# Optimization experiments

Measured on AMD Instinct MI355X. Metric: run time of the kernel, lower is better.

Reference implementation:

```python
import jax, jax.numpy as jnp
import numpy as np

IMAGE_SIZE = 128
FACES_PER_PIXEL = 4
BLUR_RADIUS = 0.01
EPS = 1e-8


def setup_inputs() -> dict:
    key = jax.random.key(0)
    k1, k2, k3 = jax.random.split(key, 3)
    B, V, F = 2, 2000, 800
    # verts are already projected to screen/NDC space: x,y in [-1,1], z > 0 (depth)
    xy = jax.random.uniform(k1, (B, V, 2), minval=-1.0, maxval=1.0)
    z = jax.random.uniform(k2, (B, V, 1), minval=0.5, maxval=2.5)
    verts = jnp.concatenate([xy, z], axis=-1).astype(jnp.float32)
    faces = jax.random.randint(k3, (F, 3), 0, V)
    return {"verts": verts, "faces": faces}


def _edge(a, b, p):
    # signed parallelogram area of (a -> b -> p), using xy components only
    return (p[..., 0] - a[..., 0]) * (b[..., 1] - a[..., 1]) - (
        p[..., 1] - a[..., 1]) * (b[..., 0] - a[..., 0])


def _seg_dist2(p, a, b):
    # squared distance from point p to segment [a, b] in 2D
    ab = b - a
    pa = p - a
    t = jnp.clip(jnp.sum(pa * ab, -1) / (jnp.sum(ab * ab, -1) + EPS), 0.0, 1.0)
    d = pa - t[..., None] * ab
    return jnp.sum(d * d, -1)


def _rasterize(verts, faces):
    H = W = IMAGE_SIZE
    K = FACES_PER_PIXEL
    B = verts.shape[0]
    fv = verts[:, faces]                      # [B,F,3,3] gather face vertices
    v0, v1, v2 = fv[:, :, 0], fv[:, :, 1], fv[:, :, 2]
    a0 = v0[:, None, :, :2]                   # [B,1,F,2]
    a1 = v1[:, None, :, :2]
    a2 = v2[:, None, :, :2]
    z0 = v0[:, None, :, 2]                    # [B,1,F]
    z1 = v1[:, None, :, 2]
    z2 = v2[:, None, :, 2]
    # pixel centers in NDC, pytorch3d convention: index 0 -> +1, last -> -1
    xs = 1.0 - 2.0 * (jnp.arange(W, dtype=verts.dtype) + 0.5) / W
    ys = 1.0 - 2.0 * (jnp.arange(H, dtype=verts.dtype) + 0.5) / H
    yy, xx = jnp.meshgrid(ys, xs, indexing="ij")
    p = jnp.stack([xx, yy], -1).reshape(1, -1, 1, 2)   # [1,P,1,2], P=H*W

    area = _edge(a0, a1, a2)                  # [B,1,F] signed face area*2
    w0 = _edge(a1, a2, p)                     # [B,P,F]
    w1 = _edge(a2, a0, p)
    w2 = _edge(a0, a1, p)
    denom = jnp.where(jnp.abs(area) > EPS, area,
                      jnp.where(area >= 0, EPS, -EPS))
    b0, b1, b2 = w0 / denom, w1 / denom, w2 / denom
    zpix = b0 * z0 + b1 * z1 + b2 * z2        # [B,P,F] interpolated depth

    inside = (b0 >= 0) & (b1 >= 0) & (b2 >= 0)
    dmin = jnp.minimum(_seg_dist2(p, a0, a1),
                       jnp.minimum(_seg_dist2(p, a1, a2),
                                   _seg_dist2(p, a2, a0)))
    dsign = jnp.where(inside, -dmin, dmin)    # signed squared edge distance

    valid = (inside | (dmin < BLUR_RADIUS)) & (zpix > EPS) & (
        jnp.abs(area) > EPS)
    zcand = jnp.where(valid, zpix, jnp.inf)
    _, idx = jax.lax.top_k(-zcand, K)         # K nearest faces per pixel

    take = lambda x: jnp.take_along_axis(x, idx, axis=-1)
    sel_valid = take(valid)
    pix_to_face = jnp.where(sel_valid, idx, -1)
    zbuf = jnp.where(sel_valid, take(zpix), -1.0)
    bary = jnp.stack([b0, b1, b2], -1)        # [B,P,F,3]
    bsel = jnp.take_along_axis(bary, idx[..., None], axis=2)  # [B,P,K,3]
    bsel = jnp.where(sel_valid[..., None], bsel, -1.0)
    dsel = jnp.where(sel_valid, take(dsign), -1.0)

    return (pix_to_face.reshape(B, H, W, K),
            zbuf.reshape(B, H, W, K),
            bsel.reshape(B, H, W, K, 3),
            dsel.reshape(B, H, W, K))


def reference(verts, faces):
    # Fragments: (pix_to_face, zbuf, bary_coords, dists)
    return _rasterize(verts, faces)
```

## Files before the change

kernel.cpp:

```cpp
#include <hip/hip_runtime.h>

#define IMG   128
#define KF    4
#define NF    800
#define NV    2000
#define NB    2
#define EPSF  1e-8f
#define BLURF 0.01f
#define CULL_D2 0.0103f
#define HEXT    0.0547f

typedef unsigned long long u64;
#define INVK ((((u64)0x7f800000u) << 32) | 0xffffffffu)

#pragma clang fp contract(off)

__device__ __forceinline__ float rcp2(float d) {
    float y = __builtin_amdgcn_rcpf(d);
    float e = __builtin_fmaf(-d, y, 1.0f);
    y = __builtin_fmaf(y, e, y);
    e = __builtin_fmaf(-d, y, 1.0f);
    y = __builtin_fmaf(y, e, y);
    return y;
}
__device__ __forceinline__ float fdivr(float n, float d, float y) {
    float q0 = n * y;
    float r  = __builtin_fmaf(-d, q0, n);
    return __builtin_fmaf(r, y, q0);
}

__device__ __forceinline__ float seg_d2(float pax, float pay, float abx, float aby) {
#pragma clang fp contract(off)
    float dd = (abx * abx + aby * aby) + EPSF;
    float t  = (pax * abx + pay * aby) / dd;
    t = fminf(fmaxf(t, 0.0f), 1.0f);
    float dx = pax - t * abx;
    float dy = pay - t * aby;
    return dx * dx + dy * dy;
}

__device__ __forceinline__ float seg_d2f(float pax, float pay, float abx, float aby) {
#pragma clang fp contract(off)
    float dd = (abx * abx + aby * aby) + EPSF;
    float n  = pax * abx + pay * aby;
    float y  = rcp2(dd);
    float t  = fdivr(n, dd, y);
    t = fminf(fmaxf(t, 0.0f), 1.0f);
    float dx = pax - t * abx;
    float dy = pay - t * aby;
    return dx * dx + dy * dy;
}

__device__ __forceinline__ void ins4(u64& s0, u64& s1, u64& s2, u64& s3, u64 k) {
    bool c0 = k < s0, c1 = k < s1, c2 = k < s2, c3 = k < s3;
    s3 = c2 ? s2 : (c3 ? k : s3);
    s2 = c1 ? s1 : (c2 ? k : s2);
    s1 = c0 ? s0 : (c1 ? k : s1);
    s0 = c0 ? k  : s0;
}

__global__ __launch_bounds__(256) void raster_p1(
    const float* __restrict__ verts,
    const int*   __restrict__ faces,
    u64* __restrict__ ws,
    int sh)
{
#pragma clang fp contract(off)
    extern __shared__ float sFD[];
    __shared__ u64 sK[2 * 4 * 64];
    __shared__ int sTot;

    const int S     = 1 << sh;
    const int chunk = NF >> sh;

    const int tid   = threadIdx.x;
    const int blk   = blockIdx.x;
    const int tile  = blk >> sh;
    const int slice = blk & (S - 1);
    const int b     = tile >> 8;
    const int trow  = (tile & 255) >> 4;
    const int tcol  = tile & 15;
    const float* vb = verts + b * NV * 3;
    const int fbase = slice * chunk;

    if (tid == 0) sTot = 0;

    const float txmax = 1.0f - (2.0f * ((float)(tcol * 8)     + 0.5f)) / 128.0f;
    const float txmin = 1.0f - (2.0f * ((float)(tcol * 8 + 7) + 0.5f)) / 128.0f;
    const float tymax = 1.0f - (2.0f * ((float)(trow * 8)     + 0.5f)) / 128.0f;
    const float tymin = 1.0f - (2.0f * ((float)(trow * 8 + 7) + 0.5f)) / 128.0f;
    const float cx = 0.5f * (txmin + txmax);
    const float cy = 0.5f * (tymin + tymax);

    __syncthreads();

    for (int j = tid; j < chunk; j += 256) {
        int f = fbase + j;
        int i0 = faces[3 * f + 0], i1 = faces[3 * f + 1], i2 = faces[3 * f + 2];
        float a0x = vb[3 * i0], a0y = vb[3 * i0 + 1], z0 = vb[3 * i0 + 2];
        float a1x = vb[3 * i1], a1y = vb[3 * i1 + 1], z1 = vb[3 * i1 + 2];
        float a2x = vb[3 * i2], a2y = vb[3 * i2 + 1], z2 = vb[3 * i2 + 2];
        float area = (a2x - a0x) * (a1y - a0y) - (a2y - a0y) * (a1x - a0x);
        bool surv = fabsf(area) > EPSF;
        float bxmin = fminf(a0x, fminf(a1x, a2x)) - 0.101f;
        float bxmax = fmaxf(a0x, fmaxf(a1x, a2x)) + 0.101f;
        float bymin = fminf(a0y, fminf(a1y, a2y)) - 0.101f;
        float bymax = fmaxf(a0y, fmaxf(a1y, a2y)) + 0.101f;
        surv &= !(bxmin > txmax || bxmax < txmin || bymin > tymax || bymax < tymin);
        float s = (area >= 0.0f) ? 1.0f : -1.0f;
        float e0x = a2x - a1x, e0y = a2y - a1y;
        float e1x = a0x - a2x, e1y = a0y - a2y;
        float e2x = a1x - a0x, e2y = a1y - a0y;
        float w0 = s * ((cx - a1x) * e0y - (cy - a1y) * e0x) + HEXT * (fabsf(e0x) + fabsf(e0y));
        float w1 = s * ((cx - a2x) * e1y - (cy - a2y) * e1x) + HEXT * (fabsf(e1x) + fabsf(e1y));
        float w2 = s * ((cx - a0x) * e2y - (cy - a0y) * e2x) + HEXT * (fabsf(e2x) + fabsf(e2y));
        float l0 = e0x * e0x + e0y * e0y;
        float l1 = e1x * e1x + e1y * e1y;
        float l2 = e2x * e2x + e2y * e2y;
        surv &= !((w0 < 0.0f) & (w0 * w0 > CULL_D2 * l0));
        surv &= !((w1 < 0.0f) & (w1 * w1 > CULL_D2 * l1));
        surv &= !((w2 < 0.0f) & (w2 * w2 > CULL_D2 * l2));
        if (surv) {
            int pos = atomicAdd(&sTot, 1);
            float* fd = &sFD[pos * 12];
            ((float4*)fd)[0] = make_float4(a0x, a0y, a1x, a1y);
            ((float4*)fd)[1] = make_float4(a2x, a2y, z0, z1);
            ((float4*)fd)[2] = make_float4(z2, area, __int_as_float(f), 0.0f);
        }
    }
    __syncthreads();
    const int total = sTot;

    const int wave = tid >> 6;
    const int lane = tid & 63;
    const int pr = lane >> 3, pc = lane & 7;
    const int row = trow * 8 + pr, col = tcol * 8 + pc;
    const float px = 1.0f - (2.0f * ((float)col + 0.5f)) / 128.0f;
    const float py = 1.0f - (2.0f * ((float)row + 0.5f)) / 128.0f;

    u64 s0 = INVK, s1 = INVK, s2 = INVK, s3 = INVK;
    for (int j = wave; j < total; j += 4) {
        const float* fd = &sFD[j * 12];
        float4 r0 = ((const float4*)fd)[0];
        float4 r1 = ((const float4*)fd)[1];
        float4 r2 = ((const float4*)fd)[2];
        float a0x = r0.x, a0y = r0.y, a1x = r0.z, a1y = r0.w;
        float a2x = r1.x, a2y = r1.y, z0 = r1.z, z1 = r1.w;
        float z2 = r2.x, denom = r2.y;
        unsigned fi = __float_as_uint(r2.z);

        float e0x = a2x - a1x, e0y = a2y - a1y;
        float e1x = a0x - a2x, e1y = a0y - a2y;
        float e2x = a1x - a0x, e2y = a1y - a0y;
        float p0x = px - a0x, p0y = py - a0y;
        float p1x = px - a1x, p1y = py - a1y;
        float p2x = px - a2x, p2y = py - a2y;
        float w0 = p1x * e0y - p1y * e0x;
        float w1 = p2x * e1y - p2y * e1x;
        float w2 = p0x * e2y - p0y * e2x;
        float y  = rcp2(denom);
        float b0 = fdivr(w0, denom, y);
        float b1 = fdivr(w1, denom, y);
        float b2 = fdivr(w2, denom, y);
        float zpix = (b0 * z0 + b1 * z1) + b2 * z2;
        bool inside = fminf(b0, fminf(b1, b2)) >= 0.0f;

        u64 okey = (zpix > EPSF) ? ((((u64)__float_as_uint(zpix)) << 32) | (u64)fi) : INVK;
        if (!__any(okey < s3)) continue;

        if (__all(inside)) {
            ins4(s0, s1, s2, s3, okey);
        } else {
            float dA = seg_d2f(p0x, p0y, e2x, e2y);
            float dB = seg_d2f(p1x, p1y, e0x, e0y);
            float dC = seg_d2f(p2x, p2y, e1x, e1y);
            float dmin = fminf(dA, fminf(dB, dC));
            u64 key = (inside | (dmin < BLURF)) ? okey : INVK;
            ins4(s0, s1, s2, s3, key);
        }
    }

    if (wave >= 2) {
        int r = wave - 2;
        sK[(r * 4 + 0) * 64 + lane] = s0;
        sK[(r * 4 + 1) * 64 + lane] = s1;
        sK[(r * 4 + 2) * 64 + lane] = s2;
        sK[(r * 4 + 3) * 64 + lane] = s3;
    }
    __syncthreads();
    if (wave < 2) {
        ins4(s0, s1, s2, s3, sK[(wave * 4 + 0) * 64 + lane]);
        ins4(s0, s1, s2, s3, sK[(wave * 4 + 1) * 64 + lane]);
        ins4(s0, s1, s2, s3, sK[(wave * 4 + 2) * 64 + lane]);
        ins4(s0, s1, s2, s3, sK[(wave * 4 + 3) * 64 + lane]);
    }
    __syncthreads();
    if (wave == 1) {
        sK[0 * 64 + lane] = s0;
        sK[1 * 64 + lane] = s1;
        sK[2 * 64 + lane] = s2;
        sK[3 * 64 + lane] = s3;
    }
    __syncthreads();
    if (wave == 0) {
        ins4(s0, s1, s2, s3, sK[0 * 64 + lane]);
        ins4(s0, s1, s2, s3, sK[1 * 64 + lane]);
        ins4(s0, s1, s2, s3, sK[2 * 64 + lane]);
        ins4(s0, s1, s2, s3, sK[3 * 64 + lane]);
        u64* wrow = ws + (size_t)blk * 256;
        wrow[0 * 64 + lane] = s0;
        wrow[1 * 64 + lane] = s1;
        wrow[2 * 64 + lane] = s2;
        wrow[3 * 64 + lane] = s3;
    }
}

__global__ __launch_bounds__(256) void raster_p2(
    const float* __restrict__ verts,
    const int*   __restrict__ faces,
    const u64* __restrict__ ws,
    int sh,
    float* __restrict__ out0, float* __restrict__ out1,
    float* __restrict__ out2, float* __restrict__ out3)
{
#pragma clang fp contract(off)
    __shared__ u64 sK[4 * 64];
    const int S    = 1 << sh;
    const int tid  = threadIdx.x;
    const int tile = blockIdx.x;
    const int b    = tile >> 8;
    const int trow = (tile & 255) >> 4;
    const int tcol = tile & 15;
    const float* vb = verts + b * NV * 3;

    if (tid < 64) {
        u64 s0 = INVK, s1 = INVK, s2 = INVK, s3 = INVK;
        const u64* base = ws + (size_t)tile * S * 256;
        for (int s = 0; s < S; ++s) {
            ins4(s0, s1, s2, s3, base[s * 256 + 0 * 64 + tid]);
            ins4(s0, s1, s2, s3, base[s * 256 + 1 * 64 + tid]);
            ins4(s0, s1, s2, s3, base[s * 256 + 2 * 64 + tid]);
            ins4(s0, s1, s2, s3, base[s * 256 + 3 * 64 + tid]);
        }
        sK[0 * 64 + tid] = s0;
        sK[1 * 64 + tid] = s1;
        sK[2 * 64 + tid] = s2;
        sK[3 * 64 + tid] = s3;
    }
    __syncthreads();

    int pix = tid >> 2, k = tid & 3;
    u64 key = sK[k * 64 + pix];
    int prow = pix >> 3, pcol = pix & 7;
    int grow = trow * 8 + prow, gcol = tcol * 8 + pcol;
    int p = (b * IMG + grow) * IMG + gcol;
    float qx = 1.0f - (2.0f * ((float)gcol + 0.5f)) / 128.0f;
    float qy = 1.0f - (2.0f * ((float)grow + 0.5f)) / 128.0f;
    float o0 = -1.0f, o1 = -1.0f, ob0 = -1.0f, ob1 = -1.0f, ob2 = -1.0f, o3 = -1.0f;
    if ((unsigned)(key >> 32) != 0x7f800000u) {
        int fi = (int)(unsigned)(key & 0xffffffffu);
        int i0 = faces[3 * fi + 0], i1 = faces[3 * fi + 1], i2 = faces[3 * fi + 2];
        float a0x = vb[3 * i0], a0y = vb[3 * i0 + 1], z0 = vb[3 * i0 + 2];
        float a1x = vb[3 * i1], a1y = vb[3 * i1 + 1], z1 = vb[3 * i1 + 2];
        float a2x = vb[3 * i2], a2y = vb[3 * i2 + 1], z2 = vb[3 * i2 + 2];
        float area = (a2x - a0x) * (a1y - a0y) - (a2y - a0y) * (a1x - a0x);
        float aab  = fabsf(area);
        float denom = (aab > EPSF) ? area : (area >= 0.0f ? EPSF : -EPSF);
        float e0x = a2x - a1x, e0y = a2y - a1y;
        float e1x = a0x - a2x, e1y = a0y - a2y;
        float e2x = a1x - a0x, e2y = a1y - a0y;
        float p0x = qx - a0x, p0y = qy - a0y;
        float p1x = qx - a1x, p1y = qy - a1y;
        float p2x = qx - a2x, p2y = qy - a2y;
        float w0 = p1x * e0y - p1y * e0x;
        float w1 = p2x * e1y - p2y * e1x;
        float w2 = p0x * e2y - p0y * e2x;
        float b0 = w0 / denom, b1 = w1 / denom, b2 = w2 / denom;
        float zpix = (b0 * z0 + b1 * z1) + b2 * z2;
        bool inside = (b0 >= 0.0f) & (b1 >= 0.0f) & (b2 >= 0.0f);
        float dA = seg_d2(p0x, p0y, e2x, e2y);
        float dB = seg_d2(p1x, p1y, e0x, e0y);
        float dC = seg_d2(p2x, p2y, e1x, e1y);
        float dmin = fminf(dA, fminf(dB, dC));
        o0 = (float)fi;
        o1 = zpix;
        ob0 = b0; ob1 = b1; ob2 = b2;
        o3 = inside ? -dmin : dmin;
    }
    int o = p * KF + k;
    out0[o] = o0;
    out1[o] = o1;
    out2[o * 3 + 0] = ob0;
    out2[o * 3 + 1] = ob1;
    out2[o * 3 + 2] = ob2;
    out3[o] = o3;
}

extern "C" void kernel_launch(void* const* d_in, const int* in_sizes, int n_in,
                              void* d_out, int out_size, void* d_ws, size_t ws_size,
                              hipStream_t stream) {
    const float* verts = (const float*)d_in[0];
    const int*   faces = (const int*)d_in[1];
    float* out = (float*)d_out;
    const int n0 = NB * IMG * IMG * KF;

    const size_t per_slice = 512ull * 256 * sizeof(u64);
    int sh;
    if      (ws_size >= 8 * per_slice) sh = 3;
    else if (ws_size >= 4 * per_slice) sh = 2;
    else if (ws_size >= 2 * per_slice) sh = 1;
    else                               sh = 0;
    const int chunk = NF >> sh;
    const size_t dyn = (size_t)chunk * 12 * sizeof(float);

    raster_p1<<<dim3(512 << sh), dim3(256), dyn, stream>>>(verts, faces, (u64*)d_ws, sh);
    raster_p2<<<dim3(512), dim3(256), 0, stream>>>(verts, faces, (const u64*)d_ws, sh,
        out,
        out + n0,
        out + 2 * n0,
        out + 5 * n0);
}
```

Before: 98.17 us.

## Precompute per-face reciprocals, prefetch face data, and refine the wave-uniform edge-distance skip

Per-face reciprocals of the signed area and of each edge's squared length are now computed once in the culling stage and stored in a wider 16-float shared record. This removes the repeated Newton reciprocal work from the per-pixel loop. The loop also software-prefetches the next face record from LDS. Edge distances are skipped whenever no lane that is outside the triangle could still enter the top-K. The maximum face split is reduced from 8 to 4 slices, which trades less parallelism in the first kernel for fewer partial lists to merge and more LDS per block.

Result: slower. 128.4 us (+30.8%).

```diff
diff --git a/kernel.cpp b/kernel.cpp
--- a/kernel.cpp
+++ b/kernel.cpp
@@ -39,11 +39,10 @@
     return dx * dx + dy * dy;
 }
 
-__device__ __forceinline__ float seg_d2f(float pax, float pay, float abx, float aby) {
+__device__ __forceinline__ float seg_d2y(float pax, float pay, float abx, float aby, float y) {
 #pragma clang fp contract(off)
     float dd = (abx * abx + aby * aby) + EPSF;
     float n  = pax * abx + pay * aby;
-    float y  = rcp2(dd);
     float t  = fdivr(n, dd, y);
     t = fminf(fmaxf(t, 0.0f), 1.0f);
     float dx = pax - t * abx;
@@ -122,10 +121,15 @@
         surv &= !((w2 < 0.0f) & (w2 * w2 > CULL_D2 * l2));
         if (surv) {
             int pos = atomicAdd(&sTot, 1);
-            float* fd = &sFD[pos * 12];
+            float yd = rcp2(area);
+            float yB = rcp2(l0 + EPSF);
+            float yC = rcp2(l1 + EPSF);
+            float yA = rcp2(l2 + EPSF);
+            float* fd = &sFD[pos * 16];
             ((float4*)fd)[0] = make_float4(a0x, a0y, a1x, a1y);
             ((float4*)fd)[1] = make_float4(a2x, a2y, z0, z1);
-            ((float4*)fd)[2] = make_float4(z2, area, __int_as_float(f), 0.0f);
+            ((float4*)fd)[2] = make_float4(z2, area, yd, __int_as_float(f));
+            ((float4*)fd)[3] = make_float4(yA, yB, yC, 0.0f);
         }
     }
     __syncthreads();
@@ -139,44 +143,55 @@
     const float py = 1.0f - (2.0f * ((float)row + 0.5f)) / 128.0f;
 
     u64 s0 = INVK, s1 = INVK, s2 = INVK, s3 = INVK;
-    for (int j = wave; j < total; j += 4) {
-        const float* fd = &sFD[j * 12];
-        float4 r0 = ((const float4*)fd)[0];
-        float4 r1 = ((const float4*)fd)[1];
-        float4 r2 = ((const float4*)fd)[2];
-        float a0x = r0.x, a0y = r0.y, a1x = r0.z, a1y = r0.w;
-        float a2x = r1.x, a2y = r1.y, z0 = r1.z, z1 = r1.w;
-        float z2 = r2.x, denom = r2.y;
-        unsigned fi = __float_as_uint(r2.z);
-
-        float e0x = a2x - a1x, e0y = a2y - a1y;
-        float e1x = a0x - a2x, e1y = a0y - a2y;
-        float e2x = a1x - a0x, e2y = a1y - a0y;
-        float p0x = px - a0x, p0y = py - a0y;
-        float p1x = px - a1x, p1y = py - a1y;
-        float p2x = px - a2x, p2y = py - a2y;
-        float w0 = p1x * e0y - p1y * e0x;
-        float w1 = p2x * e1y - p2y * e1x;
-        float w2 = p0x * e2y - p0y * e2x;
-        float y  = rcp2(denom);
-        float b0 = fdivr(w0, denom, y);
-        float b1 = fdivr(w1, denom, y);
-        float b2 = fdivr(w2, denom, y);
-        float zpix = (b0 * z0 + b1 * z1) + b2 * z2;
-        bool inside = fminf(b0, fminf(b1, b2)) >= 0.0f;
-
-        u64 okey = (zpix > EPSF) ? ((((u64)__float_as_uint(zpix)) << 32) | (u64)fi) : INVK;
-        if (!__any(okey < s3)) continue;
-
-        if (__all(inside)) {
-            ins4(s0, s1, s2, s3, okey);
-        } else {
-            float dA = seg_d2f(p0x, p0y, e2x, e2y);
-            float dB = seg_d2f(p1x, p1y, e0x, e0y);
-            float dC = seg_d2f(p2x, p2y, e1x, e1y);
-            float dmin = fminf(dA, fminf(dB, dC));
-            u64 key = (inside | (dmin < BLURF)) ? okey : INVK;
-            ins4(s0, s1, s2, s3, key);
+    if (total > 0 && wave < total) {
+        float4 q0, q1, q2, q3;
+        {
+            const float4* fp = (const float4*)&sFD[wave * 16];
+            q0 = fp[0]; q1 = fp[1]; q2 = fp[2]; q3 = fp[3];
+        }
+        for (int j = wave; j < total; ) {
+            int jn = j + 4;
+            int ja = (jn < total) ? jn : j;
+            const float4* fp = (const float4*)&sFD[ja * 16];
+            float4 n0 = fp[0], n1 = fp[1], n2 = fp[2], n3 = fp[3];
+
+            float a0x = q0.x, a0y = q0.y, a1x = q0.z, a1y = q0.w;
+            float a2x = q1.x, a2y = q1.y, z0 = q1.z, z1 = q1.w;
+            float z2 = q2.x, denom = q2.y, yd = q2.z;
+            unsigned fi = __float_as_uint(q2.w);
+            float yA = q3.x, yB = q3.y, yC = q3.z;
+
+            float e0x = a2x - a1x, e0y = a2y - a1y;
+            float e1x = a0x - a2x, e1y = a0y - a2y;
+            float e2x = a1x - a0x, e2y = a1y - a0y;
+            float p0x = px - a0x, p0y = py - a0y;
+            float p1x = px - a1x, p1y = py - a1y;
+            float p2x = px - a2x, p2y = py - a2y;
+            float w0 = p1x * e0y - p1y * e0x;
+            float w1 = p2x * e1y - p2y * e1x;
+            float w2 = p0x * e2y - p0y * e2x;
+            float b0 = fdivr(w0, denom, yd);
+            float b1 = fdivr(w1, denom, yd);
+            float b2 = fdivr(w2, denom, yd);
+            float zpix = (b0 * z0 + b1 * z1) + b2 * z2;
+            bool inside = fminf(b0, fminf(b1, b2)) >= 0.0f;
+
+            u64 okey = (zpix > EPSF) ? ((((u64)__float_as_uint(zpix)) << 32) | (u64)fi) : INVK;
+            if (__any(okey < s3)) {
+                bool need = (!inside) & (okey < s3);
+                if (!__any(need)) {
+                    ins4(s0, s1, s2, s3, inside ? okey : INVK);
+                } else {
+                    float dA = seg_d2y(p0x, p0y, e2x, e2y, yA);
+                    float dB = seg_d2y(p1x, p1y, e0x, e0y, yB);
+                    float dC = seg_d2y(p2x, p2y, e1x, e1y, yC);
+                    float dmin = fminf(dA, fminf(dB, dC));
+                    u64 key = (inside | (dmin < BLURF)) ? okey : INVK;
+                    ins4(s0, s1, s2, s3, key);
+                }
+            }
+            j = jn;
+            q0 = n0; q1 = n1; q2 = n2; q3 = n3;
         }
     }
 
@@ -306,12 +321,11 @@
 
     const size_t per_slice = 512ull * 256 * sizeof(u64);
     int sh;
-    if      (ws_size >= 8 * per_slice) sh = 3;
-    else if (ws_size >= 4 * per_slice) sh = 2;
+    if      (ws_size >= 4 * per_slice) sh = 2;
     else if (ws_size >= 2 * per_slice) sh = 1;
     else                               sh = 0;
     const int chunk = NF >> sh;
-    const size_t dyn = (size_t)chunk * 12 * sizeof(float);
+    const size_t dyn = (size_t)chunk * 16 * sizeof(float);
 
     raster_p1<<<dim3(512 << sh), dim3(256), dyn, stream>>>(verts, faces, (u64*)d_ws, sh);
     raster_p2<<<dim3(512), dim3(256), 0, stream>>>(verts, faces, (const u64*)d_ws, sh,
```

## Precompute face reciprocals in setup and add per-pixel distance cull before blur test

Applied to the files above, without the earlier changes.

Moves the reciprocal of the face area and of each squared edge length into the per-face setup stage, storing them in a wider 16-float shared record so the per-pixel loop no longer runs Newton-refined reciprocals. Adds a cheap per-pixel far-from-all-edges test, using the perpendicular distance to each edge line, that marks faces which cannot fall within the blur radius. The wave then takes the edge-distance branch only when some lane has a non-inside candidate, instead of whenever not all lanes are inside. It also caps the face-split factor at 4 rather than 8, which launches fewer first-pass blocks but gives each more faces. The wider records raise shared memory use and per-iteration LDS reads.

Result: slower. 113.4 us (+15.5%).

```diff
diff --git a/kernel.cpp b/kernel.cpp
--- a/kernel.cpp
+++ b/kernel.cpp
@@ -39,11 +39,10 @@
     return dx * dx + dy * dy;
 }
 
-__device__ __forceinline__ float seg_d2f(float pax, float pay, float abx, float aby) {
+__device__ __forceinline__ float seg_d2y(float pax, float pay, float abx, float aby, float y) {
 #pragma clang fp contract(off)
     float dd = (abx * abx + aby * aby) + EPSF;
     float n  = pax * abx + pay * aby;
-    float y  = rcp2(dd);
     float t  = fdivr(n, dd, y);
     t = fminf(fmaxf(t, 0.0f), 1.0f);
     float dx = pax - t * abx;
@@ -122,10 +121,15 @@
         surv &= !((w2 < 0.0f) & (w2 * w2 > CULL_D2 * l2));
         if (surv) {
             int pos = atomicAdd(&sTot, 1);
-            float* fd = &sFD[pos * 12];
+            float yd  = rcp2(area);
+            float ylB = rcp2(l0 + EPSF);
+            float ylC = rcp2(l1 + EPSF);
+            float ylA = rcp2(l2 + EPSF);
+            float* fd = &sFD[pos * 16];
             ((float4*)fd)[0] = make_float4(a0x, a0y, a1x, a1y);
             ((float4*)fd)[1] = make_float4(a2x, a2y, z0, z1);
-            ((float4*)fd)[2] = make_float4(z2, area, __int_as_float(f), 0.0f);
+            ((float4*)fd)[2] = make_float4(z2, area, yd, __int_as_float(f));
+            ((float4*)fd)[3] = make_float4(ylA, ylB, ylC, 0.0f);
         }
     }
     __syncthreads();
@@ -140,14 +144,16 @@
 
     u64 s0 = INVK, s1 = INVK, s2 = INVK, s3 = INVK;
     for (int j = wave; j < total; j += 4) {
-        const float* fd = &sFD[j * 12];
+        const float* fd = &sFD[j * 16];
         float4 r0 = ((const float4*)fd)[0];
         float4 r1 = ((const float4*)fd)[1];
         float4 r2 = ((const float4*)fd)[2];
+        float4 r3 = ((const float4*)fd)[3];
         float a0x = r0.x, a0y = r0.y, a1x = r0.z, a1y = r0.w;
         float a2x = r1.x, a2y = r1.y, z0 = r1.z, z1 = r1.w;
-        float z2 = r2.x, denom = r2.y;
-        unsigned fi = __float_as_uint(r2.z);
+        float z2 = r2.x, denom = r2.y, yd = r2.z;
+        unsigned fi = __float_as_uint(r2.w);
+        float ylA = r3.x, ylB = r3.y, ylC = r3.z;
 
         float e0x = a2x - a1x, e0y = a2y - a1y;
         float e1x = a0x - a2x, e1y = a0y - a2y;
@@ -158,25 +164,31 @@
         float w0 = p1x * e0y - p1y * e0x;
         float w1 = p2x * e1y - p2y * e1x;
         float w2 = p0x * e2y - p0y * e2x;
-        float y  = rcp2(denom);
-        float b0 = fdivr(w0, denom, y);
-        float b1 = fdivr(w1, denom, y);
-        float b2 = fdivr(w2, denom, y);
+        float b0 = fdivr(w0, denom, yd);
+        float b1 = fdivr(w1, denom, yd);
+        float b2 = fdivr(w2, denom, yd);
         float zpix = (b0 * z0 + b1 * z1) + b2 * z2;
         bool inside = fminf(b0, fminf(b1, b2)) >= 0.0f;
 
         u64 okey = (zpix > EPSF) ? ((((u64)__float_as_uint(zpix)) << 32) | (u64)fi) : INVK;
-        if (!__any(okey < s3)) continue;
-
-        if (__all(inside)) {
-            ins4(s0, s1, s2, s3, okey);
-        } else {
-            float dA = seg_d2f(p0x, p0y, e2x, e2y);
-            float dB = seg_d2f(p1x, p1y, e0x, e0y);
-            float dC = seg_d2f(p2x, p2y, e1x, e1y);
+
+        bool far0 = (w2 * w2) * ylA > CULL_D2;
+        bool far1 = (w0 * w0) * ylB > CULL_D2;
+        bool far2 = (w1 * w1) * ylC > CULL_D2;
+        bool mayblur = !(far0 & far1 & far2);
+
+        bool cand = (inside | mayblur) & (okey < s3);
+        if (!__any(cand)) continue;
+
+        if (__any(cand & !inside)) {
+            float dA = seg_d2y(p0x, p0y, e2x, e2y, ylA);
+            float dB = seg_d2y(p1x, p1y, e0x, e0y, ylB);
+            float dC = seg_d2y(p2x, p2y, e1x, e1y, ylC);
             float dmin = fminf(dA, fminf(dB, dC));
             u64 key = (inside | (dmin < BLURF)) ? okey : INVK;
             ins4(s0, s1, s2, s3, key);
+        } else {
+            ins4(s0, s1, s2, s3, inside ? okey : INVK);
         }
     }
 
@@ -306,12 +318,11 @@
 
     const size_t per_slice = 512ull * 256 * sizeof(u64);
     int sh;
-    if      (ws_size >= 8 * per_slice) sh = 3;
-    else if (ws_size >= 4 * per_slice) sh = 2;
+    if      (ws_size >= 4 * per_slice) sh = 2;
     else if (ws_size >= 2 * per_slice) sh = 1;
     else                               sh = 0;
     const int chunk = NF >> sh;
-    const size_t dyn = (size_t)chunk * 12 * sizeof(float);
+    const size_t dyn = (size_t)chunk * 16 * sizeof(float);
 
     raster_p1<<<dim3(512 << sh), dim3(256), dyn, stream>>>(verts, faces, (u64*)d_ws, sh);
     raster_p2<<<dim3(512), dim3(256), 0, stream>>>(verts, faces, (const u64*)d_ws, sh,
```
